# Optimization experiments

Hardware: AMD Instinct MI355X
Metric: run time of the kernel (lower is better)

Reference implementation:

```python
import jax, jax.numpy as jnp
import numpy as np

BATCH, DIM, L, N = 2, 4096, 2048, 16


def setup_inputs() -> dict:
    key = jax.random.key(0)
    ks = jax.random.split(key, 8)
    ri = lambda k, shape: jax.random.randint(k, shape, -127, 128).astype(jnp.int32)
    return {
        "u": ri(ks[0], (BATCH, DIM, L)),
        "dt": ri(ks[1], (BATCH, DIM, L)),
        "B": ri(ks[2], (BATCH, N, L)),
        "C": ri(ks[3], (BATCH, N, L)),
        "z": ri(ks[4], (BATCH, DIM, L)),
        "A_log": ri(ks[5], (DIM, N)),
        "D": ri(ks[6], (DIM,)),
        "dt_bias": ri(ks[7], (DIM,)),
        # per-tensor absmax-style scales (scalar fp32 buffers in QSScan)
        "u_scale": jnp.float32(0.01),
        "dt_scale": jnp.float32(0.004),
        "A_scale": jnp.float32(0.02),
        "B_scale": jnp.float32(0.02),
        "C_scale": jnp.float32(0.02),
        "z_scale": jnp.float32(0.02),
        "D_scale": jnp.float32(0.01),
        "dt_bias_scale": jnp.float32(0.02),
    }


def reference(u, dt, B, C, z, A_log, D, dt_bias,
              u_scale, dt_scale, A_scale, B_scale, C_scale,
              z_scale, D_scale, dt_bias_scale):
    # Dequantize INT8 operands (fused in the CUDA kernel)
    u_f = u.astype(jnp.float32) * u_scale                         # [b,d,l]
    delta = dt.astype(jnp.float32) * dt_scale \
        + (dt_bias.astype(jnp.float32) * dt_bias_scale)[None, :, None]
    delta = jax.nn.softplus(delta)                                # delta_softplus=True
    A = -jnp.exp(A_log.astype(jnp.float32) * A_scale)             # [d,n]
    B_f = B.astype(jnp.float32) * B_scale                         # [b,n,l]
    C_f = C.astype(jnp.float32) * C_scale                         # [b,n,l]

    # time-major inputs for the sequential scan
    xs = (jnp.moveaxis(delta, -1, 0),   # [l,b,d]
          jnp.moveaxis(u_f, -1, 0),     # [l,b,d]
          jnp.moveaxis(B_f, -1, 0),     # [l,b,n]
          jnp.moveaxis(C_f, -1, 0))     # [l,b,n]
    x0 = jnp.zeros((u.shape[0], u.shape[1], A.shape[1]), jnp.float32)  # [b,d,n]

    def step(x, ins):
        d_t, u_t, b_t, c_t = ins
        dA = jnp.exp(d_t[..., None] * A)                          # [b,d,n]
        x = dA * x + (d_t * u_t)[..., None] * b_t[:, None, :]     # ZOH-style discretization
        y_t = jnp.einsum('bdn,bn->bd', x, c_t)
        return x, y_t

    _, ys = jax.lax.scan(step, x0, xs)                            # [l,b,d]
    y = jnp.moveaxis(ys, 0, -1)                                   # [b,d,l]
    y = y + (D.astype(jnp.float32) * D_scale)[None, :, None] * u_f
    z_f = z.astype(jnp.float32) * z_scale
    return y * z_f * jax.nn.sigmoid(z_f)                          # gate: y * silu(z)
```

## Files before the change

### kernel.cpp

```cpp
#include <hip/hip_runtime.h>


#define LOG2E 1.44269504088896340736f
#define LN2F  0.69314718055994530942f

constexpr int BATCH = 2;
constexpr int DIM   = 4096;
constexpr int LSEQ  = 2048;
constexpr int NST   = 16;
constexpr int SCANS = BATCH * DIM;
constexpr int K     = 32;
constexpr int LC    = LSEQ / K;
constexpr int T     = 32;
constexpr int NSUB  = LC / T;
constexpr int CPB   = 2;
constexpr int SPB   = 128;
constexpr int SCOLW = 9;
constexpr int BCHS  = 648;

__device__ __forceinline__ float softplus_f(float x) {
    float e = __builtin_amdgcn_exp2f(x * LOG2E);
    return __builtin_amdgcn_logf(1.f + e) * LN2F;
}

__device__ __forceinline__ int pack8(int4 v) {
    return (v.x & 255) | ((v.y & 255) << 8) | ((v.z & 255) << 16) | ((v.w & 255) << 24);
}

#define LOAD_A2()                                                              \
    float A2[NST];                                                             \
    {                                                                          \
        const int4* ap = (const int4*)(A_log + d * NST);                       \
        int4 a0 = ap[0], a1 = ap[1], a2 = ap[2], a3 = ap[3];                   \
        const int ai[NST] = {a0.x,a0.y,a0.z,a0.w, a1.x,a1.y,a1.z,a1.w,         \
                             a2.x,a2.y,a2.z,a2.w, a3.x,a3.y,a3.z,a3.w};        \
        _Pragma("unroll")                                                      \
        for (int n = 0; n < NST; ++n)                                          \
            A2[n] = -__builtin_amdgcn_exp2f((float)ai[n] * (A_s * LOG2E)) * LOG2E; \
    }

#define STEP4(q, bt, ct)                                                       \
    {                                                                          \
        const float4 Bq = *(const float4*)((bt) + 4 * (q));                    \
        const float4 Cq = *(const float4*)((ct) + 4 * (q));                    \
        x[4*(q)+0] = __builtin_fmaf(__builtin_amdgcn_exp2f(A2[4*(q)+0] * delta), x[4*(q)+0], w * Bq.x); \
        y = __builtin_fmaf(x[4*(q)+0], Cq.x, y);                               \
        x[4*(q)+1] = __builtin_fmaf(__builtin_amdgcn_exp2f(A2[4*(q)+1] * delta), x[4*(q)+1], w * Bq.y); \
        y = __builtin_fmaf(x[4*(q)+1], Cq.y, y);                               \
        x[4*(q)+2] = __builtin_fmaf(__builtin_amdgcn_exp2f(A2[4*(q)+2] * delta), x[4*(q)+2], w * Bq.z); \
        y = __builtin_fmaf(x[4*(q)+2], Cq.z, y);                               \
        x[4*(q)+3] = __builtin_fmaf(__builtin_amdgcn_exp2f(A2[4*(q)+3] * delta), x[4*(q)+3], w * Bq.w); \
        y = __builtin_fmaf(x[4*(q)+3], Cq.w, y);                               \
    }

#define STEP4B(q, bt)                                                          \
    {                                                                          \
        const float4 Bq = *(const float4*)((bt) + 4 * (q));                    \
        x[4*(q)+0] = __builtin_fmaf(__builtin_amdgcn_exp2f(A2[4*(q)+0] * delta), x[4*(q)+0], w * Bq.x); \
        x[4*(q)+1] = __builtin_fmaf(__builtin_amdgcn_exp2f(A2[4*(q)+1] * delta), x[4*(q)+1], w * Bq.y); \
        x[4*(q)+2] = __builtin_fmaf(__builtin_amdgcn_exp2f(A2[4*(q)+2] * delta), x[4*(q)+2], w * Bq.z); \
        x[4*(q)+3] = __builtin_fmaf(__builtin_amdgcn_exp2f(A2[4*(q)+3] * delta), x[4*(q)+3], w * Bq.w); \
    }

__global__ __launch_bounds__(256, 4) void qs_phase1(
    const int* __restrict__ u,  const int* __restrict__ dt,
    const int* __restrict__ Bm, const int* __restrict__ A_log,
    const int* __restrict__ dt_bias,
    const float* __restrict__ u_sp, const float* __restrict__ dt_sp,
    const float* __restrict__ A_sp, const float* __restrict__ B_sp,
    const float* __restrict__ dtb_sp,
    float* __restrict__ Sbuf, float* __restrict__ Xbuf)
{
    const int tid = threadIdx.x;
    const int cg  = blockIdx.x >> 6;
    const int sg  = blockIdx.x & 63;
    const int scan  = sg * SPB + (tid & (SPB - 1));
    const int chunk = cg * CPB + (tid >> 7);
    const int d  = scan & (DIM - 1);
    const int bb = sg >> 5;

    __shared__ int   su_i[256 * SCOLW];
    __shared__ int   sd_i[256 * SCOLW];
    __shared__ float tB[CPB * BCHS];

    const float u_s = *u_sp, dt_s = *dt_sp, A_s = *A_sp, B_s = *B_sp, dtb_s = *dtb_sp;
    LOAD_A2();
    const float dtb = (float)dt_bias[d] * dtb_s;

    const int lr8 = tid >> 3, lo8 = tid & 7;
    const int in0 = sg * SPB * LSEQ + cg * (CPB * LC);
    const int kB  = tid & 31, nB0 = tid >> 5;
    const int bcol  = tid * (SCOLW * 4);
    const int tbase = (tid >> 7) * BCHS;

    float x[NST];
#pragma unroll
    for (int n = 0; n < NST; ++n) x[n] = 0.f;
    float S = 0.f;

    for (int st = 0; st < NSUB; ++st) {
        const int c0 = st * T;
#pragma unroll
        for (int p = 0; p < 8; ++p) {
            const int seg = p * 32 + lr8;
            const int ga  = in0 + (seg & (SPB - 1)) * LSEQ + (seg >> 7) * LC + c0 + 4 * lo8;
            su_i[seg * SCOLW + lo8] = pack8(*(const int4*)(u  + ga));
            sd_i[seg * SCOLW + lo8] = pack8(*(const int4*)(dt + ga));
        }
#pragma unroll
        for (int j = 0; j < CPB; ++j)
#pragma unroll
            for (int j2 = 0; j2 < 2; ++j2) {
                const int n = nB0 + 8 * j2;
                tB[j * BCHS + kB * 20 + n] =
                    (float)Bm[(bb * NST + n) * LSEQ + cg * (CPB * LC) + j * LC + c0 + kB];
            }
        __syncthreads();

        const signed char* suc = (const signed char*)su_i;
        const signed char* sdc = (const signed char*)sd_i;
#pragma unroll 4
        for (int k = 0; k < T; ++k) {
            const float uf    = (float)suc[bcol + k] * u_s;
            const float delta = softplus_f((float)sdc[bcol + k] * dt_s + dtb);
            const float w     = delta * uf * B_s;
            S += delta;
            const float* bt = &tB[tbase + k * 20];
            STEP4B(0, bt); STEP4B(1, bt); STEP4B(2, bt); STEP4B(3, bt);
        }
        __syncthreads();
    }

    Sbuf[chunk * SCANS + scan] = S;
    float4* Xo = (float4*)(Xbuf + (chunk * SCANS + scan) * NST);
#pragma unroll
    for (int q = 0; q < 4; ++q)
        Xo[q] = make_float4(x[4*q], x[4*q+1], x[4*q+2], x[4*q+3]);
}

__global__ __launch_bounds__(256) void qs_combine(
    const int* __restrict__ A_log, const float* __restrict__ A_sp,
    const float* __restrict__ Sbuf, float* __restrict__ Xbuf)
{
    const int idx  = blockIdx.x * 256 + threadIdx.x;
    const int scan = idx >> 4, n = idx & 15;
    const int d    = scan & (DIM - 1);
    const float A2 = -__builtin_amdgcn_exp2f(
        (float)A_log[d * NST + n] * ((*A_sp) * LOG2E)) * LOG2E;
    float x = 0.f;
#pragma unroll
    for (int c = 0; c < K; ++c) {
        const int off = c * (SCANS * NST) + idx;
        const float Xe = Xbuf[off];
        const float P  = __builtin_amdgcn_exp2f(A2 * Sbuf[c * SCANS + scan]);
        Xbuf[off] = x;
        x = __builtin_fmaf(P, x, Xe);
    }
}

__global__ __launch_bounds__(256, 4) void qs_phase2(
    const int* __restrict__ u,  const int* __restrict__ dt,
    const int* __restrict__ Bm, const int* __restrict__ Cm,
    const int* __restrict__ z,  const int* __restrict__ A_log,
    const int* __restrict__ Dv, const int* __restrict__ dt_bias,
    const float* __restrict__ u_sp,  const float* __restrict__ dt_sp,
    const float* __restrict__ A_sp,  const float* __restrict__ B_sp,
    const float* __restrict__ C_sp,  const float* __restrict__ z_sp,
    const float* __restrict__ D_sp,  const float* __restrict__ dtb_sp,
    const float* __restrict__ XI, float* __restrict__ out)
{
    const int tid = threadIdx.x;
    const int cg  = blockIdx.x >> 6;
    const int sg  = blockIdx.x & 63;
    const int scan  = sg * SPB + (tid & (SPB - 1));
    const int chunk = cg * CPB + (tid >> 7);
    const int d  = scan & (DIM - 1);
    const int bb = sg >> 5;

    __shared__ int   su_i[256 * SCOLW];
    __shared__ int   sd_i[256 * SCOLW];
    __shared__ int   sz_i[256 * SCOLW];
    __shared__ float tB[CPB * BCHS];
    __shared__ float tC[CPB * BCHS];

    const float u_s = *u_sp, dt_s = *dt_sp, A_s = *A_sp, B_s = *B_sp;
    const float C_s = *C_sp, z_s  = *z_sp,  D_s = *D_sp, dtb_s = *dtb_sp;
    LOAD_A2();
    const float dtb = (float)dt_bias[d] * dtb_s;
    const float Dd  = (float)Dv[d] * D_s;

    float x[NST];
    {
        const float4* xi = (const float4*)(XI + (chunk * SCANS + scan) * NST);
        const float4 x0 = xi[0], x1 = xi[1], x2 = xi[2], x3 = xi[3];
        x[0]=x0.x; x[1]=x0.y; x[2]=x0.z; x[3]=x0.w;
        x[4]=x1.x; x[5]=x1.y; x[6]=x1.z; x[7]=x1.w;
        x[8]=x2.x; x[9]=x2.y; x[10]=x2.z; x[11]=x2.w;
        x[12]=x3.x; x[13]=x3.y; x[14]=x3.z; x[15]=x3.w;
    }

    const int lr8 = tid >> 3, lo8 = tid & 7;
    const int in0 = sg * SPB * LSEQ + cg * (CPB * LC);
    const int kB  = tid & 31, nB0 = tid >> 5;
    const int bcol  = tid * (SCOLW * 4);
    const int tbase = (tid >> 7) * BCHS;
    const int ob = scan * LSEQ + chunk * LC;

    for (int st = 0; st < NSUB; ++st) {
        const int c0 = st * T;
#pragma unroll
        for (int p = 0; p < 8; ++p) {
            const int seg = p * 32 + lr8;
            const int ga  = in0 + (seg & (SPB - 1)) * LSEQ + (seg >> 7) * LC + c0 + 4 * lo8;
            su_i[seg * SCOLW + lo8] = pack8(*(const int4*)(u  + ga));
            sd_i[seg * SCOLW + lo8] = pack8(*(const int4*)(dt + ga));
            sz_i[seg * SCOLW + lo8] = pack8(*(const int4*)(z  + ga));
        }
#pragma unroll
        for (int j = 0; j < CPB; ++j)
#pragma unroll
            for (int j2 = 0; j2 < 2; ++j2) {
                const int n  = nB0 + 8 * j2;
                const int gr = (bb * NST + n) * LSEQ + cg * (CPB * LC) + j * LC + c0 + kB;
                tB[j * BCHS + kB * 20 + n] = (float)Bm[gr];
                tC[j * BCHS + kB * 20 + n] = (float)Cm[gr];
            }
        __syncthreads();

        const signed char* suc = (const signed char*)su_i;
        const signed char* sdc = (const signed char*)sd_i;
        const signed char* szc = (const signed char*)sz_i;
        float ya[16];
#pragma unroll 4
        for (int k = 0; k < T; ++k) {
            const float uf    = (float)suc[bcol + k] * u_s;
            const float delta = softplus_f((float)sdc[bcol + k] * dt_s + dtb);
            const float w     = delta * uf * B_s;
            const float zf    = (float)szc[bcol + k] * z_s;
            const float gate  = zf * __builtin_amdgcn_rcpf(
                                    1.f + __builtin_amdgcn_exp2f(-zf * LOG2E));
            const float* bt = &tB[tbase + k * 20];
            const float* ct = &tC[tbase + k * 20];
            float y = 0.f;
            STEP4(0, bt, ct); STEP4(1, bt, ct); STEP4(2, bt, ct); STEP4(3, bt, ct);
            ya[k & 15] = __builtin_fmaf(y, C_s, Dd * uf) * gate;
            if ((k & 15) == 15) {
                float* ob2 = out + ob + c0 + (k - 15);
#pragma unroll
                for (int q = 0; q < 4; ++q)
                    *(float4*)(ob2 + 4 * q) =
                        make_float4(ya[4*q], ya[4*q+1], ya[4*q+2], ya[4*q+3]);
            }
        }
        __syncthreads();
    }
}

extern "C" void kernel_launch(void* const* d_in, const int* in_sizes, int n_in,
                              void* d_out, int out_size, void* d_ws, size_t ws_size,
                              hipStream_t stream) {
    const int* u   = (const int*)d_in[0];
    const int* dt  = (const int*)d_in[1];
    const int* Bm  = (const int*)d_in[2];
    const int* Cm  = (const int*)d_in[3];
    const int* z   = (const int*)d_in[4];
    const int* Al  = (const int*)d_in[5];
    const int* Dv  = (const int*)d_in[6];
    const int* dtb = (const int*)d_in[7];
    const float* u_sp = (const float*)d_in[8],  * dt_sp = (const float*)d_in[9];
    const float* A_sp = (const float*)d_in[10], * B_sp  = (const float*)d_in[11];
    const float* C_sp = (const float*)d_in[12], * z_sp  = (const float*)d_in[13];
    const float* D_sp = (const float*)d_in[14], * dtb_sp= (const float*)d_in[15];

    float* Xbuf = (float*)d_ws;
    float* Sbuf = Xbuf + (size_t)K * SCANS * NST;

    dim3 blk(256);
    qs_phase1<<<dim3(16 * 64), blk, 0, stream>>>(u, dt, Bm, Al, dtb,
        u_sp, dt_sp, A_sp, B_sp, dtb_sp, Sbuf, Xbuf);
    qs_combine<<<dim3(SCANS * NST / 256), blk, 0, stream>>>(Al, A_sp, Sbuf, Xbuf);
    qs_phase2<<<dim3(16 * 64), blk, 0, stream>>>(u, dt, Bm, Cm, z, Al, Dv, dtb,
        u_sp, dt_sp, A_sp, B_sp, C_sp, z_sp, D_sp, dtb_sp, Xbuf, (float*)d_out);
}
```

Before: 150.6 us.

## Double chunk count to 64 and process one 32-step chunk per block

Raises the number of sequence chunks from 32 to 64 so each chunk is 32 steps long. Each block now covers 256 scans of a single chunk, loaded to shared memory in one pass, which drops the inner sub-tile loop and its extra barriers. The combine kernel does twice as many sequential steps and the intermediate state buffer doubles in size, adding memory traffic. The combine loop unroll is also reduced to 8.

```diff
diff --git a/kernel.cpp b/kernel.cpp
--- a/kernel.cpp
+++ b/kernel.cpp
@@ -9,14 +9,10 @@
 constexpr int LSEQ  = 2048;
 constexpr int NST   = 16;
 constexpr int SCANS = BATCH * DIM;
-constexpr int K     = 32;
+constexpr int K     = 64;
 constexpr int LC    = LSEQ / K;
-constexpr int T     = 32;
-constexpr int NSUB  = LC / T;
-constexpr int CPB   = 2;
-constexpr int SPB   = 128;
-constexpr int SCOLW = 9;
-constexpr int BCHS  = 648;
+constexpr int SPB   = 256;
+constexpr int NSG   = SCANS / SPB;
 
 __device__ __forceinline__ float softplus_f(float x) {
     float e = __builtin_amdgcn_exp2f(x * LOG2E);
@@ -72,67 +68,56 @@
     float* __restrict__ Sbuf, float* __restrict__ Xbuf)
 {
     const int tid = threadIdx.x;
-    const int cg  = blockIdx.x >> 6;
-    const int sg  = blockIdx.x & 63;
-    const int scan  = sg * SPB + (tid & (SPB - 1));
-    const int chunk = cg * CPB + (tid >> 7);
+    const int cg  = blockIdx.x >> 5;
+    const int sg  = blockIdx.x & 31;
+    const int scan = sg * SPB + tid;
     const int d  = scan & (DIM - 1);
-    const int bb = sg >> 5;
-
-    __shared__ int   su_i[256 * SCOLW];
-    __shared__ int   sd_i[256 * SCOLW];
-    __shared__ float tB[CPB * BCHS];
+    const int bb = sg >> 4;
+
+    __shared__ int   sud[256 * 17];
+    __shared__ float tB[LC * 20];
 
     const float u_s = *u_sp, dt_s = *dt_sp, A_s = *A_sp, B_s = *B_sp, dtb_s = *dtb_sp;
     LOAD_A2();
     const float dtb = (float)dt_bias[d] * dtb_s;
 
-    const int lr8 = tid >> 3, lo8 = tid & 7;
-    const int in0 = sg * SPB * LSEQ + cg * (CPB * LC);
+    const int lc8 = tid >> 3, lo8 = tid & 7;
+    const int in0 = sg * SPB * LSEQ + cg * LC;
     const int kB  = tid & 31, nB0 = tid >> 5;
-    const int bcol  = tid * (SCOLW * 4);
-    const int tbase = (tid >> 7) * BCHS;
+    const int bcol = tid * 68;
+
+#pragma unroll
+    for (int p = 0; p < 8; ++p) {
+        const int col = p * 32 + lc8;
+        const int ga  = in0 + col * LSEQ + 4 * lo8;
+        sud[col * 17 + lo8]     = pack8(*(const int4*)(u  + ga));
+        sud[col * 17 + 8 + lo8] = pack8(*(const int4*)(dt + ga));
+    }
+#pragma unroll
+    for (int j2 = 0; j2 < 2; ++j2) {
+        const int n = nB0 + 8 * j2;
+        tB[kB * 20 + n] = (float)Bm[(bb * NST + n) * LSEQ + cg * LC + kB];
+    }
+    __syncthreads();
 
     float x[NST];
 #pragma unroll
     for (int n = 0; n < NST; ++n) x[n] = 0.f;
     float S = 0.f;
 
-    for (int st = 0; st < NSUB; ++st) {
-        const int c0 = st * T;
-#pragma unroll
-        for (int p = 0; p < 8; ++p) {
-            const int seg = p * 32 + lr8;
-            const int ga  = in0 + (seg & (SPB - 1)) * LSEQ + (seg >> 7) * LC + c0 + 4 * lo8;
-            su_i[seg * SCOLW + lo8] = pack8(*(const int4*)(u  + ga));
-            sd_i[seg * SCOLW + lo8] = pack8(*(const int4*)(dt + ga));
-        }
-#pragma unroll
-        for (int j = 0; j < CPB; ++j)
-#pragma unroll
-            for (int j2 = 0; j2 < 2; ++j2) {
-                const int n = nB0 + 8 * j2;
-                tB[j * BCHS + kB * 20 + n] =
-                    (float)Bm[(bb * NST + n) * LSEQ + cg * (CPB * LC) + j * LC + c0 + kB];
-            }
-        __syncthreads();
-
-        const signed char* suc = (const signed char*)su_i;
-        const signed char* sdc = (const signed char*)sd_i;
+    const signed char* sc = (const signed char*)sud;
 #pragma unroll 4
-        for (int k = 0; k < T; ++k) {
-            const float uf    = (float)suc[bcol + k] * u_s;
-            const float delta = softplus_f((float)sdc[bcol + k] * dt_s + dtb);
-            const float w     = delta * uf * B_s;
-            S += delta;
-            const float* bt = &tB[tbase + k * 20];
-            STEP4B(0, bt); STEP4B(1, bt); STEP4B(2, bt); STEP4B(3, bt);
-        }
-        __syncthreads();
-    }
-
-    Sbuf[chunk * SCANS + scan] = S;
-    float4* Xo = (float4*)(Xbuf + (chunk * SCANS + scan) * NST);
+    for (int k = 0; k < LC; ++k) {
+        const float uf    = (float)sc[bcol + k] * u_s;
+        const float delta = softplus_f((float)sc[bcol + 32 + k] * dt_s + dtb);
+        const float w     = delta * uf * B_s;
+        S += delta;
+        const float* bt = &tB[k * 20];
+        STEP4B(0, bt); STEP4B(1, bt); STEP4B(2, bt); STEP4B(3, bt);
+    }
+
+    Sbuf[cg * SCANS + scan] = S;
+    float4* Xo = (float4*)(Xbuf + (cg * SCANS + scan) * NST);
 #pragma unroll
     for (int q = 0; q < 4; ++q)
         Xo[q] = make_float4(x[4*q], x[4*q+1], x[4*q+2], x[4*q+3]);
@@ -148,7 +133,7 @@
     const float A2 = -__builtin_amdgcn_exp2f(
         (float)A_log[d * NST + n] * ((*A_sp) * LOG2E)) * LOG2E;
     float x = 0.f;
-#pragma unroll
+#pragma unroll 8
     for (int c = 0; c < K; ++c) {
         const int off = c * (SCANS * NST) + idx;
         const float Xe = Xbuf[off];
@@ -170,18 +155,15 @@
     const float* __restrict__ XI, float* __restrict__ out)
 {
     const int tid = threadIdx.x;
-    const int cg  = blockIdx.x >> 6;
-    const int sg  = blockIdx.x & 63;
-    const int scan  = sg * SPB + (tid & (SPB - 1));
-    const int chunk = cg * CPB + (tid >> 7);
+    const int cg  = blockIdx.x >> 5;
+    const int sg  = blockIdx.x & 31;
+    const int scan = sg * SPB + tid;
     const int d  = scan & (DIM - 1);
-    const int bb = sg >> 5;
-
-    __shared__ int   su_i[256 * SCOLW];
-    __shared__ int   sd_i[256 * SCOLW];
-    __shared__ int   sz_i[256 * SCOLW];
-    __shared__ float tB[CPB * BCHS];
-    __shared__ float tC[CPB * BCHS];
+    const int bb = sg >> 4;
+
+    __shared__ int   suz[256 * 25];
+    __shared__ float tB[LC * 20];
+    __shared__ float tC[LC * 20];
 
     const float u_s = *u_sp, dt_s = *dt_sp, A_s = *A_sp, B_s = *B_sp;
     const float C_s = *C_sp, z_s  = *z_sp,  D_s = *D_sp, dtb_s = *dtb_sp;
@@ -191,7 +173,7 @@
 
     float x[NST];
     {
-        const float4* xi = (const float4*)(XI + (chunk * SCANS + scan) * NST);
+        const float4* xi = (const float4*)(XI + (cg * SCANS + scan) * NST);
         const float4 x0 = xi[0], x1 = xi[1], x2 = xi[2], x3 = xi[3];
         x[0]=x0.x; x[1]=x0.y; x[2]=x0.z; x[3]=x0.w;
         x[4]=x1.x; x[5]=x1.y; x[6]=x1.z; x[7]=x1.w;
@@ -199,60 +181,51 @@
         x[12]=x3.x; x[13]=x3.y; x[14]=x3.z; x[15]=x3.w;
     }
 
-    const int lr8 = tid >> 3, lo8 = tid & 7;
-    const int in0 = sg * SPB * LSEQ + cg * (CPB * LC);
+    const int lc8 = tid >> 3, lo8 = tid & 7;
+    const int in0 = sg * SPB * LSEQ + cg * LC;
     const int kB  = tid & 31, nB0 = tid >> 5;
-    const int bcol  = tid * (SCOLW * 4);
-    const int tbase = (tid >> 7) * BCHS;
-    const int ob = scan * LSEQ + chunk * LC;
-
-    for (int st = 0; st < NSUB; ++st) {
-        const int c0 = st * T;
-#pragma unroll
-        for (int p = 0; p < 8; ++p) {
-            const int seg = p * 32 + lr8;
-            const int ga  = in0 + (seg & (SPB - 1)) * LSEQ + (seg >> 7) * LC + c0 + 4 * lo8;
-            su_i[seg * SCOLW + lo8] = pack8(*(const int4*)(u  + ga));
-            sd_i[seg * SCOLW + lo8] = pack8(*(const int4*)(dt + ga));
-            sz_i[seg * SCOLW + lo8] = pack8(*(const int4*)(z  + ga));
+    const int bcol = tid * 100;
+    const int ob   = scan * LSEQ + cg * LC;
+
+#pragma unroll
+    for (int p = 0; p < 8; ++p) {
+        const int col = p * 32 + lc8;
+        const int ga  = in0 + col * LSEQ + 4 * lo8;
+        suz[col * 25 + lo8]      = pack8(*(const int4*)(u  + ga));
+        suz[col * 25 + 8 + lo8]  = pack8(*(const int4*)(dt + ga));
+        suz[col * 25 + 16 + lo8] = pack8(*(const int4*)(z  + ga));
+    }
+#pragma unroll
+    for (int j2 = 0; j2 < 2; ++j2) {
+        const int n  = nB0 + 8 * j2;
+        const int gr = (bb * NST + n) * LSEQ + cg * LC + kB;
+        tB[kB * 20 + n] = (float)Bm[gr];
+        tC[kB * 20 + n] = (float)Cm[gr];
+    }
+    __syncthreads();
+
+    const signed char* sc = (const signed char*)suz;
+    float ya[16];
+#pragma unroll 4
+    for (int k = 0; k < LC; ++k) {
+        const float uf    = (float)sc[bcol + k] * u_s;
+        const float delta = softplus_f((float)sc[bcol + 32 + k] * dt_s + dtb);
+        const float w     = delta * uf * B_s;
+        const float zf    = (float)sc[bcol + 64 + k] * z_s;
+        const float gate  = zf * __builtin_amdgcn_rcpf(
+                                1.f + __builtin_amdgcn_exp2f(-zf * LOG2E));
+        const float* bt = &tB[k * 20];
+        const float* ct = &tC[k * 20];
+        float y = 0.f;
+        STEP4(0, bt, ct); STEP4(1, bt, ct); STEP4(2, bt, ct); STEP4(3, bt, ct);
+        ya[k & 15] = __builtin_fmaf(y, C_s, Dd * uf) * gate;
+        if ((k & 15) == 15) {
+            float* ob2 = out + ob + (k - 15);
+#pragma unroll
+            for (int q = 0; q < 4; ++q)
+                *(float4*)(ob2 + 4 * q) =
+                    make_float4(ya[4*q], ya[4*q+1], ya[4*q+2], ya[4*q+3]);
         }
-#pragma unroll
-        for (int j = 0; j < CPB; ++j)
-#pragma unroll
-            for (int j2 = 0; j2 < 2; ++j2) {
-                const int n  = nB0 + 8 * j2;
-                const int gr = (bb * NST + n) * LSEQ + cg * (CPB * LC) + j * LC + c0 + kB;
-                tB[j * BCHS + kB * 20 + n] = (float)Bm[gr];
-                tC[j * BCHS + kB * 20 + n] = (float)Cm[gr];
-            }
-        __syncthreads();
-
-        const signed char* suc = (const signed char*)su_i;
-        const signed char* sdc = (const signed char*)sd_i;
-        const signed char* szc = (const signed char*)sz_i;
-        float ya[16];
-#pragma unroll 4
-        for (int k = 0; k < T; ++k) {
-            const float uf    = (float)suc[bcol + k] * u_s;
-            const float delta = softplus_f((float)sdc[bcol + k] * dt_s + dtb);
-            const float w     = delta * uf * B_s;
-            const float zf    = (float)szc[bcol + k] * z_s;
-            const float gate  = zf * __builtin_amdgcn_rcpf(
-                                    1.f + __builtin_amdgcn_exp2f(-zf * LOG2E));
-            const float* bt = &tB[tbase + k * 20];
-            const float* ct = &tC[tbase + k * 20];
-            float y = 0.f;
-            STEP4(0, bt, ct); STEP4(1, bt, ct); STEP4(2, bt, ct); STEP4(3, bt, ct);
-            ya[k & 15] = __builtin_fmaf(y, C_s, Dd * uf) * gate;
-            if ((k & 15) == 15) {
-                float* ob2 = out + ob + c0 + (k - 15);
-#pragma unroll
-                for (int q = 0; q < 4; ++q)
-                    *(float4*)(ob2 + 4 * q) =
-                        make_float4(ya[4*q], ya[4*q+1], ya[4*q+2], ya[4*q+3]);
-            }
-        }
-        __syncthreads();
     }
 }
 
@@ -276,9 +249,9 @@
     float* Sbuf = Xbuf + (size_t)K * SCANS * NST;
 
     dim3 blk(256);
-    qs_phase1<<<dim3(16 * 64), blk, 0, stream>>>(u, dt, Bm, Al, dtb,
+    qs_phase1<<<dim3(K * NSG), blk, 0, stream>>>(u, dt, Bm, Al, dtb,
         u_sp, dt_sp, A_sp, B_sp, dtb_sp, Sbuf, Xbuf);
     qs_combine<<<dim3(SCANS * NST / 256), blk, 0, stream>>>(Al, A_sp, Sbuf, Xbuf);
-    qs_phase2<<<dim3(16 * 64), blk, 0, stream>>>(u, dt, Bm, Cm, z, Al, Dv, dtb,
+    qs_phase2<<<dim3(K * NSG), blk, 0, stream>>>(u, dt, Bm, Cm, z, Al, Dv, dtb,
         u_sp, dt_sp, A_sp, B_sp, C_sp, z_sp, D_sp, dtb_sp, Xbuf, (float*)d_out);
 }
```

After: 149.6 us, median of 2. Within noise of the previous version (-0.7%).
